# Kernel optimization log

Measured on AMD Instinct MI355X. Metric: run time of the kernel, lower is better.

Reference implementation:

```python
import jax, jax.numpy as jnp
import numpy as np
import math

B, N, C = 8, 2048, 512

def setup_inputs() -> dict:
    key = jax.random.key(0)
    ks = jax.random.split(key, 7)
    s = 1.0 / math.sqrt(C)
    return {
        "feature": jax.random.normal(ks[0], (B, N, C), dtype=jnp.float32),
        "wq": jax.random.uniform(ks[1], (C, C), jnp.float32, -s, s),
        "bq": jax.random.uniform(ks[2], (C,), jnp.float32, -s, s),
        "wk": jax.random.uniform(ks[3], (C, C), jnp.float32, -s, s),
        "bk": jax.random.uniform(ks[4], (C,), jnp.float32, -s, s),
        "wv": jax.random.uniform(ks[5], (C, C), jnp.float32, -s, s),
        "bv": jax.random.uniform(ks[6], (C,), jnp.float32, -s, s),
    }

def reference(feature, wq, bq, wk, bk, wv, bv):
    # torch nn.Linear: x @ W.T + b
    q = jnp.einsum('bnc,dc->bnd', feature, wq) + bq
    k = jnp.einsum('bnc,dc->bnd', feature, wk) + bk
    v = jnp.einsum('bnc,dc->bnd', feature, wv) + bv
    scores = jnp.einsum('bnd,bmd->bnm', q, k)          # [B, N, N]
    attn = jax.nn.softmax(scores, axis=2) / math.sqrt(C)  # post-softmax scale (as in source)
    v_star = jnp.einsum('bnm,bmd->bnd', attn, v)
    return feature + v_star
```

## Files before the change

kernel.cpp:

```cpp
#include <hip/hip_runtime.h>
#include <cstdint>
#include <cstddef>


typedef __bf16 bf16x8 __attribute__((ext_vector_type(8)));
typedef float f32x4 __attribute__((ext_vector_type(4)));
typedef short short4v __attribute__((ext_vector_type(4)));

__device__ __forceinline__ short f2b(float f) {
  union { float f; unsigned u; } u; u.f = f;
  unsigned r = (u.u + 0x7fffu + ((u.u >> 16) & 1u)) >> 16;
  return (short)r;
}

#define GLDS(gptr, lptr) \
  __builtin_amdgcn_global_load_lds( \
      (const __attribute__((address_space(1))) unsigned int*)(const void*)(gptr), \
      (__attribute__((address_space(3))) unsigned int*)(void*)(lptr), 16, 0, 0)

__device__ __forceinline__ bf16x8 ldfrag64(const short* buf, int row, int kq) {
  return *(const bf16x8*)(buf + row * 64 + ((kq ^ (row & 7)) * 8));
}

__device__ __forceinline__ bf16x8 ldfrag_a(const short* buf, int row, int kq) {
  const short* p = buf + row * 64 + ((kq ^ (row & 7)) * 8);
  bf16x8 r;
  asm volatile("ds_read_b128 %0, %1"
               : "=v"(r)
               : "v"((const __attribute__((address_space(3))) short*)(const void*)p));
  return r;
}

#define LGKM0_SB() do { \
    asm volatile("s_waitcnt lgkmcnt(0)" ::: "memory"); \
    __builtin_amdgcn_sched_barrier(0); } while (0)
#define VMW(n) asm volatile("s_waitcnt vmcnt(" #n ")" ::: "memory")
#define SBAR() __builtin_amdgcn_s_barrier()
#define PRIO1() __builtin_amdgcn_s_setprio(1)
#define PRIO0() __builtin_amdgcn_s_setprio(0)

__device__ __forceinline__ void ldA4(bf16x8 (&a)[4][2], const short* buf, int rb, int l4) {
#pragma unroll
  for (int j = 0; j < 4; ++j)
#pragma unroll
    for (int kk = 0; kk < 2; ++kk) a[j][kk] = ldfrag_a(buf, rb + j * 16, kk * 4 + l4);
}
__device__ __forceinline__ void ld2(bf16x8 (&b)[2][2], const short* buf, int rb, int l4) {
#pragma unroll
  for (int n = 0; n < 2; ++n)
#pragma unroll
    for (int kk = 0; kk < 2; ++kk) b[n][kk] = ldfrag_a(buf, rb + n * 16, kk * 4 + l4);
}
__device__ __forceinline__ void mm42(f32x4 (&acc)[8][4], const bf16x8 (&a)[4][2],
                                     const bf16x8 (&b)[2][2], int io, int no) {
#pragma unroll
  for (int kk = 0; kk < 2; ++kk)
#pragma unroll
    for (int j = 0; j < 4; ++j)
#pragma unroll
      for (int n = 0; n < 2; ++n)
        acc[io + j][no + n] = __builtin_amdgcn_mfma_f32_16x16x32_bf16(
            a[j][kk], b[n][kk], acc[io + j][no + n], 0, 0, 0);
}
__device__ __forceinline__ void mm22(f32x4 (&acc)[4][4], const bf16x8 (&a)[2][2],
                                     const bf16x8 (&b)[2][2], int io, int no) {
#pragma unroll
  for (int kk = 0; kk < 2; ++kk)
#pragma unroll
    for (int j = 0; j < 2; ++j)
#pragma unroll
      for (int n = 0; n < 2; ++n)
        acc[io + j][no + n] = __builtin_amdgcn_mfma_f32_16x16x32_bf16(
            a[j][kk], b[n][kk], acc[io + j][no + n], 0, 0, 0);
}

__global__ __launch_bounds__(256) void prep(const float* __restrict__ f,
                                            const float* __restrict__ w0,
                                            const float* __restrict__ w1,
                                            const float* __restrict__ w2,
                                            const float* __restrict__ b0,
                                            const float* __restrict__ b1,
                                            const float* __restrict__ b2,
                                            short* __restrict__ Xb, short* __restrict__ Wb,
                                            float* __restrict__ biasP, float* __restrict__ l) {
  const int bid = blockIdx.x;
  const int t = threadIdx.x;
  if (bid < 8192) {
    int i = bid * 256 + t;
    float4 v = ((const float4*)f)[i];
    short4v o = { f2b(v.x), f2b(v.y), f2b(v.z), f2b(v.w) };
    *(short4v*)(Xb + (size_t)i * 4) = o;
  } else if (bid < 8960) {
    int i = (bid - 8192) * 256 + t;
    const float* src = (i < 65536) ? w0 : (i < 131072) ? w1 : w2;
    float4 v = ((const float4*)src)[i & 65535];
    short4v o = { f2b(v.x), f2b(v.y), f2b(v.z), f2b(v.w) };
    *(short4v*)(Wb + (size_t)i * 4) = o;
  } else {
    int i = (bid - 8960) * 256 + t;
    float4 z = { 0.f, 0.f, 0.f, 0.f };
    ((float4*)l)[i * 2] = z;
    ((float4*)l)[i * 2 + 1] = z;
    if (i < 1536) {
      const float* s = (i < 512) ? b0 : (i < 1024) ? b1 : b2;
      biasP[i] = s[i & 511];
    }
  }
}

__global__ __launch_bounds__(256) void gemm_qkv(const short* __restrict__ X,
                                                const short* __restrict__ Wall,
                                                const float* __restrict__ biasP,
                                                short* __restrict__ Out,
                                                short* __restrict__ VtOut) {
  __shared__ __align__(16) short Xs[128 * 64];
  __shared__ __align__(16) short Ws[128 * 64];
  const int z = blockIdx.z;
  const short* Wm = Wall + (size_t)z * 262144;
  const int m0 = blockIdx.y * 128, n0 = blockIdx.x * 128;
  const int t = threadIdx.x;
  const int lane = t & 63, w = t >> 6;
  const int wn = (w & 1) * 64, wm = (w >> 1) * 64;
  const int fr = lane & 15, l4 = lane >> 4;

  f32x4 acc[4][4] = {};

  for (int k0 = 0; k0 < 512; k0 += 64) {
    __syncthreads();
#pragma unroll
    for (int u = 0; u < 4; ++u) {
      int cc = t + u * 256;
      int r = cc >> 3, cs = cc & 7;
      int kk = ((cs ^ (r & 7)) * 8);
      GLDS(X + (size_t)(m0 + r) * 512 + k0 + kk, Xs + cc * 8);
      GLDS(Wm + (size_t)(n0 + r) * 512 + k0 + kk, Ws + cc * 8);
    }
    __syncthreads();
#pragma unroll
    for (int h = 0; h < 2; ++h) {
      bf16x8 wf[4], xf[4];
#pragma unroll
      for (int i = 0; i < 4; ++i) wf[i] = ldfrag64(Ws, wn + i * 16 + fr, h * 4 + l4);
#pragma unroll
      for (int j = 0; j < 4; ++j) xf[j] = ldfrag64(Xs, wm + j * 16 + fr, h * 4 + l4);
      if (z < 2) {
#pragma unroll
        for (int i = 0; i < 4; ++i)
#pragma unroll
          for (int j = 0; j < 4; ++j)
            acc[i][j] = __builtin_amdgcn_mfma_f32_16x16x32_bf16(wf[i], xf[j], acc[i][j], 0, 0, 0);
      } else {
#pragma unroll
        for (int i = 0; i < 4; ++i)
#pragma unroll
          for (int j = 0; j < 4; ++j)
            acc[i][j] = __builtin_amdgcn_mfma_f32_16x16x32_bf16(xf[i], wf[j], acc[i][j], 0, 0, 0);
      }
    }
  }

  const int rq = l4 * 4;
  if (z < 2) {
#pragma unroll
    for (int i = 0; i < 4; ++i) {
      int nb = n0 + wn + i * 16 + rq;
      float4 bs = *(const float4*)(biasP + z * 512 + nb);
#pragma unroll
      for (int j = 0; j < 4; ++j) {
        int m = m0 + wm + j * 16 + fr;
        short4v o = { f2b(acc[i][j][0] + bs.x), f2b(acc[i][j][1] + bs.y),
                      f2b(acc[i][j][2] + bs.z), f2b(acc[i][j][3] + bs.w) };
        *(short4v*)(Out + (size_t)z * 8388608 + (size_t)m * 512 + nb) = o;
      }
    }
  } else {
    const int zB = blockIdx.y >> 4;
    const int mb = m0 & 2047;
#pragma unroll
    for (int j = 0; j < 4; ++j) {
      int d = n0 + wn + j * 16 + fr;
      float bd = biasP[1024 + d];
#pragma unroll
      for (int i = 0; i < 4; ++i) {
        int mloc = mb + wm + i * 16 + rq;
        short4v o = { f2b(acc[i][j][0] + bd), f2b(acc[i][j][1] + bd),
                      f2b(acc[i][j][2] + bd), f2b(acc[i][j][3] + bd) };
        *(short4v*)(VtOut + (size_t)zB * 1048576 + (size_t)d * 2048 + mloc) = o;
      }
    }
  }
}

__global__ __launch_bounds__(512, 2) void gemm_qk8(const short* __restrict__ Q,
                                                   const short* __restrict__ Kb,
                                                   short* __restrict__ P,
                                                   float* __restrict__ l) {
  __shared__ __align__(16) short As[2][16384];
  __shared__ __align__(16) short Bs[2][16384];
  const int id = blockIdx.x + blockIdx.y * 8 + blockIdx.z * 64;
  const int swz = (id & 7) * 64 + (id >> 3);
  const int z = swz >> 6;
  const int m0 = ((swz >> 3) & 7) * 256;
  const int n0 = (swz & 7) * 256;
  const short* __restrict__ A = Kb + (size_t)z * 1048576;
  const short* __restrict__ B = Q + (size_t)z * 1048576;
  const int t = threadIdx.x;
  const int lane = t & 63, w = t >> 6;
  const int aw = (w >> 2) * 64, bw = (w & 3) * 32;
  const int fr = lane & 15, l4 = lane >> 4;
  const int r0 = t >> 3;
  const int kswz = ((t & 7) ^ (r0 & 7)) * 8;
  const short* pA = A + (size_t)(m0 + r0) * 512 + kswz;
  const short* pB = B + (size_t)(n0 + r0) * 512 + kswz;

#define QK_STG_A(buf, h, kt) do { \
    GLDS(pA + (size_t)((h) * 128) * 512 + (kt) * 64, &As[(buf)][(h) * 8192 + t * 8]); \
    GLDS(pA + (size_t)((h) * 128 + 64) * 512 + (kt) * 64, &As[(buf)][(h) * 8192 + 4096 + t * 8]); \
  } while (0)
#define QK_STG_B(buf, h, kt) do { \
    GLDS(pB + (size_t)((h) * 128) * 512 + (kt) * 64, &Bs[(buf)][(h) * 8192 + t * 8]); \
    GLDS(pB + (size_t)((h) * 128 + 64) * 512 + (kt) * 64, &Bs[(buf)][(h) * 8192 + 4096 + t * 8]); \
  } while (0)

  f32x4 acc[8][4] = {};

  QK_STG_A(0, 0, 0); QK_STG_B(0, 0, 0); QK_STG_B(0, 1, 0); QK_STG_A(0, 1, 0);
  QK_STG_A(1, 0, 1); QK_STG_B(1, 0, 1); QK_STG_B(1, 1, 1);
  VMW(6);
  SBAR();

  bf16x8 af[4][2], b0[2][2], b1[2][2];
  for (int kt = 0; kt < 6; ++kt) {
    const int c = kt & 1;
    const short* Ac = &As[c][0];
    const short* Bc = &Bs[c][0];
    ldA4(af, Ac, aw + fr, l4); ld2(b0, Bc, bw + fr, l4);
    QK_STG_A(c ^ 1, 1, kt + 1);
    SBAR(); LGKM0_SB(); PRIO1(); mm42(acc, af, b0, 0, 0); PRIO0(); SBAR();
    ld2(b1, Bc, 128 + bw + fr, l4);
    QK_STG_A(c, 0, kt + 2);
    SBAR(); LGKM0_SB(); PRIO1(); mm42(acc, af, b1, 0, 2); PRIO0(); SBAR();
    ldA4(af, Ac, 128 + aw + fr, l4);
    QK_STG_B(c, 0, kt + 2);
    SBAR(); LGKM0_SB(); PRIO1(); mm42(acc, af, b1, 4, 2); PRIO0(); SBAR();
    QK_STG_B(c, 1, kt + 2);
    VMW(6);
    SBAR(); PRIO1(); mm42(acc, af, b0, 4, 0); PRIO0(); SBAR();
  }
  {
    const short *Ac = &As[0][0], *Bc = &Bs[0][0];
    ldA4(af, Ac, aw + fr, l4); ld2(b0, Bc, bw + fr, l4);
    QK_STG_A(1, 1, 7);
    SBAR(); LGKM0_SB(); PRIO1(); mm42(acc, af, b0, 0, 0); PRIO0(); SBAR();
    ld2(b1, Bc, 128 + bw + fr, l4);
    SBAR(); LGKM0_SB(); PRIO1(); mm42(acc, af, b1, 0, 2); PRIO0(); SBAR();
    ldA4(af, Ac, 128 + aw + fr, l4);
    SBAR(); LGKM0_SB(); PRIO1(); mm42(acc, af, b1, 4, 2); PRIO0(); SBAR();
    VMW(0);
    SBAR(); PRIO1(); mm42(acc, af, b0, 4, 0); PRIO0(); SBAR();
  }
  {
    const short *Ac = &As[1][0], *Bc = &Bs[1][0];
    ldA4(af, Ac, aw + fr, l4); ld2(b0, Bc, bw + fr, l4);
    SBAR(); LGKM0_SB(); PRIO1(); mm42(acc, af, b0, 0, 0); PRIO0(); SBAR();
    ld2(b1, Bc, 128 + bw + fr, l4);
    SBAR(); LGKM0_SB(); PRIO1(); mm42(acc, af, b1, 0, 2); PRIO0(); SBAR();
    ldA4(af, Ac, 128 + aw + fr, l4);
    SBAR(); LGKM0_SB(); PRIO1(); mm42(acc, af, b1, 4, 2); PRIO0();
    mm42(acc, af, b0, 4, 0);
  }
#undef QK_STG_A
#undef QK_STG_B

  const float LOG2E = 1.4426950408889634f;
  float rs[4] = { 0.f, 0.f, 0.f, 0.f };
#pragma unroll
  for (int i = 0; i < 8; ++i) {
    const int key = m0 + aw + (i & 3) * 16 + (i >> 2) * 128 + l4 * 4;
#pragma unroll
    for (int n = 0; n < 4; ++n) {
      const int q = n0 + bw + (n & 1) * 16 + (n >> 1) * 128 + fr;
      short4v o;
      float part = 0.f;
#pragma unroll
      for (int r = 0; r < 4; ++r) {
        float e = exp2f(acc[i][n][r] * LOG2E);
        o[r] = f2b(e);
        part += e;
      }
      *(short4v*)(P + (size_t)z * 4194304 + (size_t)q * 2048 + key) = o;
      rs[n] += part;
    }
  }
#pragma unroll
  for (int n = 0; n < 4; ++n) {
    rs[n] += __shfl_xor(rs[n], 16);
    rs[n] += __shfl_xor(rs[n], 32);
  }
  if (l4 == 0) {
#pragma unroll
    for (int n = 0; n < 4; ++n)
      atomicAdd(&l[z * 2048 + n0 + bw + (n & 1) * 16 + (n >> 1) * 128 + fr], rs[n]);
  }
}

__global__ __launch_bounds__(512, 2) void gemm_pv8(const short* __restrict__ Pm,
                                                   const short* __restrict__ Vt,
                                                   const float* __restrict__ l,
                                                   const float* __restrict__ resid,
                                                   float* __restrict__ out, float scale) {
  __shared__ __align__(16) short As[2][8192];
  __shared__ __align__(16) short Bs[2][16384];
  const int id = blockIdx.x + blockIdx.y * 4 + blockIdx.z * 32;
  const int swz = (id & 7) * 32 + (id >> 3);
  const int z = swz >> 5;
  const int d0 = (swz & 3) * 128;
  const int n0 = ((swz >> 2) & 7) * 256;
  const short* __restrict__ A = Vt + (size_t)z * 1048576;
  const short* __restrict__ B = Pm + (size_t)z * 4194304;
  const int t = threadIdx.x;
  const int lane = t & 63, w = t >> 6;
  const int aw = (w >> 2) * 32, bw = (w & 3) * 32;
  const int fr = lane & 15, l4 = lane >> 4;
  const int r0 = t >> 3;
  const int kswz = ((t & 7) ^ (r0 & 7)) * 8;
  const short* pA = A + (size_t)(d0 + r0) * 2048 + kswz;
  const short* pB = B + (size_t)(n0 + r0) * 2048 + kswz;

#define PV_STG_A(buf, h, kt) \
    GLDS(pA + (size_t)((h) * 64) * 2048 + (kt) * 64, &As[(buf)][(h) * 4096 + t * 8])
#define PV_STG_B(buf, h, kt) do { \
    GLDS(pB + (size_t)((h) * 128) * 2048 + (kt) * 64, &Bs[(buf)][(h) * 8192 + t * 8]); \
    GLDS(pB + (size_t)((h) * 128 + 64) * 2048 + (kt) * 64, &Bs[(buf)][(h) * 8192 + 4096 + t * 8]); \
  } while (0)

  f32x4 acc[4][4] = {};

  PV_STG_A(0, 0, 0); PV_STG_B(0, 0, 0); PV_STG_B(0, 1, 0); PV_STG_A(0, 1, 0);
  PV_STG_A(1, 0, 1); PV_STG_B(1, 0, 1); PV_STG_B(1, 1, 1);
  VMW(5);
  SBAR();

  bf16x8 a[2][2], b0[2][2], b1[2][2];
  for (int kt = 0; kt < 30; ++kt) {
    const int c = kt & 1;
    const short* Ac = &As[c][0];
    const short* Bc = &Bs[c][0];
    ld2(a, Ac, aw + fr, l4); ld2(b0, Bc, bw + fr, l4); ld2(b1, Bc, 128 + bw + fr, l4);
    PV_STG_A(c ^ 1, 1, kt + 1);
    SBAR(); LGKM0_SB(); PRIO1();
    mm22(acc, a, b0, 0, 0); mm22(acc, a, b1, 0, 2);
    PRIO0(); SBAR();
    ld2(a, Ac, 64 + aw + fr, l4);
    PV_STG_A(c, 0, kt + 2);
    PV_STG_B(c, 0, kt + 2);
    PV_STG_B(c, 1, kt + 2);
    VMW(5);
    SBAR(); LGKM0_SB(); PRIO1();
    mm22(acc, a, b1, 2, 2); mm22(acc, a, b0, 2, 0);
    PRIO0(); SBAR();
  }
  {
    const short *Ac = &As[0][0], *Bc = &Bs[0][0];
    ld2(a, Ac, aw + fr, l4); ld2(b0, Bc, bw + fr, l4); ld2(b1, Bc, 128 + bw + fr, l4);
    PV_STG_A(1, 1, 31);
    SBAR(); LGKM0_SB(); PRIO1();
    mm22(acc, a, b0, 0, 0); mm22(acc, a, b1, 0, 2);
    PRIO0(); SBAR();
    ld2(a, Ac, 64 + aw + fr, l4);
    VMW(0);
    SBAR(); LGKM0_SB(); PRIO1();
    mm22(acc, a, b1, 2, 2); mm22(acc, a, b0, 2, 0);
    PRIO0(); SBAR();
  }
  {
    const short *Ac = &As[1][0], *Bc = &Bs[1][0];
    ld2(a, Ac, aw + fr, l4); ld2(b0, Bc, bw + fr, l4); ld2(b1, Bc, 128 + bw + fr, l4);
    SBAR(); LGKM0_SB(); PRIO1();
    mm22(acc, a, b0, 0, 0); mm22(acc, a, b1, 0, 2);
    PRIO0(); SBAR();
    ld2(a, Ac, 64 + aw + fr, l4);
    LGKM0_SB(); PRIO1();
    mm22(acc, a, b1, 2, 2); mm22(acc, a, b0, 2, 0);
    PRIO0();
  }
#undef PV_STG_A
#undef PV_STG_B

  float linv[4];
#pragma unroll
  for (int n = 0; n < 4; ++n) {
    const int q = n0 + bw + (n & 1) * 16 + (n >> 1) * 128 + fr;
    linv[n] = scale / l[z * 2048 + q];
  }
#pragma unroll
  for (int n = 0; n < 4; ++n) {
    const int q = n0 + bw + (n & 1) * 16 + (n >> 1) * 128 + fr;
#pragma unroll
    for (int i = 0; i < 4; ++i) {
      const int d = d0 + aw + (i & 1) * 16 + (i >> 1) * 64 + l4 * 4;
      const size_t idx = (size_t)z * 1048576 + (size_t)q * 512 + d;
      float4 rv = *(const float4*)(resid + idx);
      float4 o = { rv.x + acc[i][n][0] * linv[n], rv.y + acc[i][n][1] * linv[n],
                   rv.z + acc[i][n][2] * linv[n], rv.w + acc[i][n][3] * linv[n] };
      *(float4*)(out + idx) = o;
    }
  }
}

extern "C" void kernel_launch(void* const* d_in, const int* in_sizes, int n_in,
                              void* d_out, int out_size, void* d_ws, size_t ws_size,
                              hipStream_t stream) {
  const float* feature = (const float*)d_in[0];
  const float* wq = (const float*)d_in[1];
  const float* bq = (const float*)d_in[2];
  const float* wk = (const float*)d_in[3];
  const float* bk = (const float*)d_in[4];
  const float* wv = (const float*)d_in[5];
  const float* bv = (const float*)d_in[6];
  float* out = (float*)d_out;

  const size_t MN = (size_t)16384 * 512;
  short* Xb = (short*)d_ws;
  short* Wb = Xb + MN;
  short* Q = Wb + 786432;
  short* K = Q + MN;
  short* Vt = K + MN;
  short* P = Vt + MN;
  float* biasP = (float*)(P + (size_t)8 * 2048 * 2048);
  float* l = biasP + 1536;

  prep<<<8968, 256, 0, stream>>>(feature, wq, wk, wv, bq, bk, bv, Xb, Wb, biasP, l);

  gemm_qkv<<<dim3(4, 128, 3), 256, 0, stream>>>(Xb, Wb, biasP, Q, Vt);
  gemm_qk8<<<dim3(8, 8, 8), 512, 0, stream>>>(Q, K, P, l);

  const float iscl = 0.044194173824159216f;
  gemm_pv8<<<dim3(4, 8, 8), 512, 0, stream>>>(P, Vt, l, feature, out, iscl);
}
```

Before: 229.9 us.

## Rewrite QKV projection GEMM with 256x256 tiles and double-buffered pipelined loads

```diff
diff --git a/kernel.cpp b/kernel.cpp
--- a/kernel.cpp
+++ b/kernel.cpp
@@ -17,10 +17,6 @@
   __builtin_amdgcn_global_load_lds( \
       (const __attribute__((address_space(1))) unsigned int*)(const void*)(gptr), \
       (__attribute__((address_space(3))) unsigned int*)(void*)(lptr), 16, 0, 0)
-
-__device__ __forceinline__ bf16x8 ldfrag64(const short* buf, int row, int kq) {
-  return *(const bf16x8*)(buf + row * 64 + ((kq ^ (row & 7)) * 8));
-}
 
 __device__ __forceinline__ bf16x8 ldfrag_a(const short* buf, int row, int kq) {
   const short* p = buf + row * 64 + ((kq ^ (row & 7)) * 8);
@@ -108,83 +104,116 @@
   }
 }
 
-__global__ __launch_bounds__(256) void gemm_qkv(const short* __restrict__ X,
-                                                const short* __restrict__ Wall,
-                                                const float* __restrict__ biasP,
-                                                short* __restrict__ Out,
-                                                short* __restrict__ VtOut) {
-  __shared__ __align__(16) short Xs[128 * 64];
-  __shared__ __align__(16) short Ws[128 * 64];
-  const int z = blockIdx.z;
-  const short* Wm = Wall + (size_t)z * 262144;
-  const int m0 = blockIdx.y * 128, n0 = blockIdx.x * 128;
+__global__ __launch_bounds__(512, 2) void gemm_qkv256(const short* __restrict__ X,
+                                                      const short* __restrict__ Wall,
+                                                      const float* __restrict__ biasP,
+                                                      short* __restrict__ Out,
+                                                      short* __restrict__ VtOut) {
+  __shared__ __align__(16) short As[2][16384];
+  __shared__ __align__(16) short Bs[2][16384];
+  const int id = blockIdx.x + blockIdx.y * 2 + blockIdx.z * 128;
+  const int swz = (id & 7) * 48 + (id >> 3);
+  const int z = swz >> 7;
+  const int rem = swz & 127;
+  const int m0 = (rem >> 1) * 256;
+  const int n0 = (rem & 1) * 256;
+  const short* __restrict__ Wm = Wall + (size_t)z * 262144 + (size_t)n0 * 512;
+  const short* __restrict__ Xm = X + (size_t)m0 * 512;
+  const short* __restrict__ Ag = (z < 2) ? Wm : Xm;
+  const short* __restrict__ Bg = (z < 2) ? Xm : Wm;
   const int t = threadIdx.x;
   const int lane = t & 63, w = t >> 6;
-  const int wn = (w & 1) * 64, wm = (w >> 1) * 64;
+  const int aw = (w >> 2) * 64, bw = (w & 3) * 32;
   const int fr = lane & 15, l4 = lane >> 4;
-
-  f32x4 acc[4][4] = {};
-
-  for (int k0 = 0; k0 < 512; k0 += 64) {
-    __syncthreads();
-#pragma unroll
-    for (int u = 0; u < 4; ++u) {
-      int cc = t + u * 256;
-      int r = cc >> 3, cs = cc & 7;
-      int kk = ((cs ^ (r & 7)) * 8);
-      GLDS(X + (size_t)(m0 + r) * 512 + k0 + kk, Xs + cc * 8);
-      GLDS(Wm + (size_t)(n0 + r) * 512 + k0 + kk, Ws + cc * 8);
-    }
-    __syncthreads();
-#pragma unroll
-    for (int h = 0; h < 2; ++h) {
-      bf16x8 wf[4], xf[4];
-#pragma unroll
-      for (int i = 0; i < 4; ++i) wf[i] = ldfrag64(Ws, wn + i * 16 + fr, h * 4 + l4);
-#pragma unroll
-      for (int j = 0; j < 4; ++j) xf[j] = ldfrag64(Xs, wm + j * 16 + fr, h * 4 + l4);
-      if (z < 2) {
-#pragma unroll
-        for (int i = 0; i < 4; ++i)
-#pragma unroll
-          for (int j = 0; j < 4; ++j)
-            acc[i][j] = __builtin_amdgcn_mfma_f32_16x16x32_bf16(wf[i], xf[j], acc[i][j], 0, 0, 0);
-      } else {
-#pragma unroll
-        for (int i = 0; i < 4; ++i)
-#pragma unroll
-          for (int j = 0; j < 4; ++j)
-            acc[i][j] = __builtin_amdgcn_mfma_f32_16x16x32_bf16(xf[i], wf[j], acc[i][j], 0, 0, 0);
-      }
-    }
-  }
-
-  const int rq = l4 * 4;
+  const int r0 = t >> 3;
+  const int kswz = ((t & 7) ^ (r0 & 7)) * 8;
+  const short* pA = Ag + (size_t)r0 * 512 + kswz;
+  const short* pB = Bg + (size_t)r0 * 512 + kswz;
+
+#define QV_STG_A(buf, h, kt) do { \
+    GLDS(pA + (size_t)((h) * 128) * 512 + (kt) * 64, &As[(buf)][(h) * 8192 + t * 8]); \
+    GLDS(pA + (size_t)((h) * 128 + 64) * 512 + (kt) * 64, &As[(buf)][(h) * 8192 + 4096 + t * 8]); \
+  } while (0)
+#define QV_STG_B(buf, h, kt) do { \
+    GLDS(pB + (size_t)((h) * 128) * 512 + (kt) * 64, &Bs[(buf)][(h) * 8192 + t * 8]); \
+    GLDS(pB + (size_t)((h) * 128 + 64) * 512 + (kt) * 64, &Bs[(buf)][(h) * 8192 + 4096 + t * 8]); \
+  } while (0)
+
+  f32x4 acc[8][4] = {};
+
+  QV_STG_A(0, 0, 0); QV_STG_B(0, 0, 0); QV_STG_B(0, 1, 0); QV_STG_A(0, 1, 0);
+  QV_STG_A(1, 0, 1); QV_STG_B(1, 0, 1); QV_STG_B(1, 1, 1);
+  VMW(6);
+  SBAR();
+
+  bf16x8 af[4][2], b0[2][2], b1[2][2];
+  for (int kt = 0; kt < 6; ++kt) {
+    const int c = kt & 1;
+    const short* Ac = &As[c][0];
+    const short* Bc = &Bs[c][0];
+    ldA4(af, Ac, aw + fr, l4); ld2(b0, Bc, bw + fr, l4);
+    QV_STG_A(c ^ 1, 1, kt + 1);
+    SBAR(); LGKM0_SB(); PRIO1(); mm42(acc, af, b0, 0, 0); PRIO0(); SBAR();
+    ld2(b1, Bc, 128 + bw + fr, l4);
+    QV_STG_A(c, 0, kt + 2);
+    SBAR(); LGKM0_SB(); PRIO1(); mm42(acc, af, b1, 0, 2); PRIO0(); SBAR();
+    ldA4(af, Ac, 128 + aw + fr, l4);
+    QV_STG_B(c, 0, kt + 2);
+    SBAR(); LGKM0_SB(); PRIO1(); mm42(acc, af, b1, 4, 2); PRIO0(); SBAR();
+    QV_STG_B(c, 1, kt + 2);
+    VMW(6);
+    SBAR(); PRIO1(); mm42(acc, af, b0, 4, 0); PRIO0(); SBAR();
+  }
+  {
+    const short *Ac = &As[0][0], *Bc = &Bs[0][0];
+    ldA4(af, Ac, aw + fr, l4); ld2(b0, Bc, bw + fr, l4);
+    QV_STG_A(1, 1, 7);
+    SBAR(); LGKM0_SB(); PRIO1(); mm42(acc, af, b0, 0, 0); PRIO0(); SBAR();
+    ld2(b1, Bc, 128 + bw + fr, l4);
+    SBAR(); LGKM0_SB(); PRIO1(); mm42(acc, af, b1, 0, 2); PRIO0(); SBAR();
+    ldA4(af, Ac, 128 + aw + fr, l4);
+    SBAR(); LGKM0_SB(); PRIO1(); mm42(acc, af, b1, 4, 2); PRIO0(); SBAR();
+    VMW(0);
+    SBAR(); PRIO1(); mm42(acc, af, b0, 4, 0); PRIO0(); SBAR();
+  }
+  {
+    const short *Ac = &As[1][0], *Bc = &Bs[1][0];
+    ldA4(af, Ac, aw + fr, l4); ld2(b0, Bc, bw + fr, l4);
+    SBAR(); LGKM0_SB(); PRIO1(); mm42(acc, af, b0, 0, 0); PRIO0(); SBAR();
+    ld2(b1, Bc, 128 + bw + fr, l4);
+    SBAR(); LGKM0_SB(); PRIO1(); mm42(acc, af, b1, 0, 2); PRIO0(); SBAR();
+    ldA4(af, Ac, 128 + aw + fr, l4);
+    SBAR(); LGKM0_SB(); PRIO1(); mm42(acc, af, b1, 4, 2); PRIO0();
+    mm42(acc, af, b0, 4, 0);
+  }
+#undef QV_STG_A
+#undef QV_STG_B
+
   if (z < 2) {
 #pragma unroll
-    for (int i = 0; i < 4; ++i) {
-      int nb = n0 + wn + i * 16 + rq;
+    for (int i = 0; i < 8; ++i) {
+      const int nb = n0 + aw + (i & 3) * 16 + (i >> 2) * 128 + l4 * 4;
       float4 bs = *(const float4*)(biasP + z * 512 + nb);
 #pragma unroll
-      for (int j = 0; j < 4; ++j) {
-        int m = m0 + wm + j * 16 + fr;
-        short4v o = { f2b(acc[i][j][0] + bs.x), f2b(acc[i][j][1] + bs.y),
-                      f2b(acc[i][j][2] + bs.z), f2b(acc[i][j][3] + bs.w) };
+      for (int n = 0; n < 4; ++n) {
+        const int m = m0 + bw + (n & 1) * 16 + (n >> 1) * 128 + fr;
+        short4v o = { f2b(acc[i][n][0] + bs.x), f2b(acc[i][n][1] + bs.y),
+                      f2b(acc[i][n][2] + bs.z), f2b(acc[i][n][3] + bs.w) };
         *(short4v*)(Out + (size_t)z * 8388608 + (size_t)m * 512 + nb) = o;
       }
     }
   } else {
-    const int zB = blockIdx.y >> 4;
+    const int zB = m0 >> 11;
     const int mb = m0 & 2047;
 #pragma unroll
-    for (int j = 0; j < 4; ++j) {
-      int d = n0 + wn + j * 16 + fr;
-      float bd = biasP[1024 + d];
-#pragma unroll
-      for (int i = 0; i < 4; ++i) {
-        int mloc = mb + wm + i * 16 + rq;
-        short4v o = { f2b(acc[i][j][0] + bd), f2b(acc[i][j][1] + bd),
-                      f2b(acc[i][j][2] + bd), f2b(acc[i][j][3] + bd) };
+    for (int n = 0; n < 4; ++n) {
+      const int d = n0 + bw + (n & 1) * 16 + (n >> 1) * 128 + fr;
+      const float bd = biasP[1024 + d];
+#pragma unroll
+      for (int i = 0; i < 8; ++i) {
+        const int mloc = mb + aw + (i & 3) * 16 + (i >> 2) * 128 + l4 * 4;
+        short4v o = { f2b(acc[i][n][0] + bd), f2b(acc[i][n][1] + bd),
+                      f2b(acc[i][n][2] + bd), f2b(acc[i][n][3] + bd) };
         *(short4v*)(VtOut + (size_t)zB * 1048576 + (size_t)d * 2048 + mloc) = o;
       }
     }
@@ -432,7 +461,7 @@
 
   prep<<<8968, 256, 0, stream>>>(feature, wq, wk, wv, bq, bk, bv, Xb, Wb, biasP, l);
 
-  gemm_qkv<<<dim3(4, 128, 3), 256, 0, stream>>>(Xb, Wb, biasP, Q, Vt);
+  gemm_qkv256<<<dim3(2, 64, 3), 512, 0, stream>>>(Xb, Wb, biasP, Q, Vt);
   gemm_qk8<<<dim3(8, 8, 8), 512, 0, stream>>>(Q, K, P, l);
 
   const float iscl = 0.044194173824159216f;
```

After: 230.4 us. About the same (+0.2%).
